# Performance work log

Hardware: AMD Instinct MI355X
Metric: run time of the kernel (lower is better)

The kernel has to match this reference:

```python
import jax, jax.numpy as jnp
import numpy as np

# Config matching init_kwargs: input_shape=(512,512,28), stride=2
M, N, L = 512, 512, 28
STRIDE = 2
B = 8


def setup_inputs() -> dict:
    key = jax.random.key(0)
    kx, kp = jax.random.split(key)
    x = jax.random.normal(kx, (B, L, M, N), dtype=jnp.float32)
    # phi = (1 + sign(randn)) / 2  -> binary {0,1} mask of shape (M, N)
    phi = (jax.random.normal(kp, (M, N)) > 0).astype(jnp.float32)
    return {"x": x, "phi": phi}


def reference(x, phi):
    """CASSI forward: get_transpose(get_measurement(x, phi), phi, mask_mul=True).

    x:   (b, L, M, N) hyperspectral cube
    phi: (M, N) coded aperture, broadcast across L bands
    """
    b, l, m, n = x.shape
    n_out = n + STRIDE * (l - 1)

    # --- get_measurement: mask-multiply then per-band shift-and-accumulate ---
    y1 = x * phi[None, None, :, :]                      # (b, L, M, N)
    # column index each (band, col) lands in after dispersion shift
    scat_idx = (STRIDE * jnp.arange(l)[:, None] + jnp.arange(n)[None, :]).reshape(-1)  # (L*N,)
    y1f = y1.transpose(0, 2, 1, 3).reshape(b, m, l * n)  # (b, M, L*N)
    y2 = jnp.zeros((b, m, n_out), dtype=x.dtype).at[:, :, scat_idx].add(y1f)  # (b, M, Nout)
    # y_norm=False: no normalization

    # --- get_transpose: gather shifted windows (width = y.shape[-2] = M) ---
    gat_idx = STRIDE * jnp.arange(l)[:, None] + jnp.arange(m)[None, :]  # (L, M)
    xt = y2[:, :, gat_idx]             # (b, M, L, M)
    xt = jnp.moveaxis(xt, 2, 1)        # (b, L, M, M)
    return xt * phi[None, None, :, :]  # mask_mul=True
```

## Files before the change

### kernel.cpp

```cpp
#include <hip/hip_runtime.h>


#define M_DIM 512
#define N_DIM 512
#define L_DIM 28
#define B_DIM 8
#define MN_DIM (M_DIM * N_DIM)
#define NT 14
#define U_DIM 14

typedef float v2f __attribute__((ext_vector_type(2)));
typedef float v4f __attribute__((ext_vector_type(4)));

__global__ __launch_bounds__(256) void cassi_fwd_kernel(
    const float* __restrict__ x, const float* __restrict__ phi,
    float* __restrict__ out)
{
    __shared__ __align__(16) float sphi[2][N_DIM];
    __shared__ __align__(16) float sy2[2][576];

    const int tid = threadIdx.x;
    const int r   = tid >> 7;
    const int t   = tid & 127;
    const int bm  = blockIdx.x;
    const int b   = bm >> 8;
    const int m   = ((bm & 255) << 1) | r;

    const float* xrow = x + (size_t)b * L_DIM * MN_DIM + (size_t)m * N_DIM;

    v4f pq = *(const v4f*)(phi + (size_t)m * N_DIM + 4 * t);
    *(v4f*)&sphi[r][4 * t] = pq;
    __syncthreads();

    const float* sphif = &sphi[r][0];
    const bool lane0 = ((tid & 63) == 0);

    v4f acc  = {0.f, 0.f, 0.f, 0.f};
    v4f acct = {0.f, 0.f, 0.f, 0.f};

#pragma unroll
    for (int u = 0; u < U_DIM; ++u) {
        const int s  = t - u;
        const int sc = s < 0 ? 0 : s;
        const float* re = xrow + (size_t)(2 * u) * MN_DIM;
        const float* ro = xrow + (size_t)(2 * u + 1) * MN_DIM;
        v4f xe = *(const v4f*)(re + 4 * sc);
        v4f xo = *(const v4f*)(ro + 4 * sc);
        v4f P  = *(const v4f*)(sphif + 4 * sc);
        v4f ze = xe * P;
        v4f zo = xo * P;

        if (s >= 0) acc += ze;

        float lo0 = __shfl_up(zo.z, 1, 64);
        float lo1 = __shfl_up(zo.w, 1, 64);
        if (lane0 && s >= 1) {
            v2f xl = *(const v2f*)(ro + 4 * s - 2);
            v2f pl = *(const v2f*)(sphif + 4 * s - 2);
            lo0 = xl.x * pl.x;
            lo1 = xl.y * pl.y;
        }
        if (s >= 1) { acc.x += lo0;  acc.y += lo1; }
        if (s >= 0) { acc.z += zo.x; acc.w += zo.y; }

        if (t < NT) {
            if (u == t) {
                v2f xl = *(const v2f*)(ro + 510);
                v2f pl = *(const v2f*)(sphif + 510);
                acct.x += xl.x * pl.x;
                acct.y += xl.y * pl.y;
            } else if (u > t) {
                const int n0 = 512 + 4 * t - 4 * u;
                v4f xte = *(const v4f*)(re + n0);
                v4f Pt  = *(const v4f*)(sphif + n0);
                acct += xte * Pt;
                v2f xa = *(const v2f*)(ro + n0 - 2);
                v2f pa = *(const v2f*)(sphif + n0 - 2);
                v2f xb = *(const v2f*)(ro + n0);
                acct.x += xa.x * pa.x;
                acct.y += xa.y * pa.y;
                acct.z += xb.x * Pt.x;
                acct.w += xb.y * Pt.y;
            }
        }
    }

    *(v4f*)&sy2[r][4 * t] = acc;
    if (t < NT) *(v4f*)&sy2[r][512 + 4 * t] = acct;
    __syncthreads();

    float* orow = out + (size_t)b * L_DIM * MN_DIM + (size_t)m * N_DIM;
    const float* sy = &sy2[r][0];
#pragma unroll
    for (int l = 0; l < L_DIM; ++l) {
        v2f ya = *(const v2f*)(sy + 2 * l + 4 * t);
        v2f yb = *(const v2f*)(sy + 2 * l + 4 * t + 2);
        v4f o;
        o.x = pq.x * ya.x;
        o.y = pq.y * ya.y;
        o.z = pq.z * yb.x;
        o.w = pq.w * yb.y;
        __builtin_nontemporal_store(o, (v4f*)(orow + (size_t)l * MN_DIM + 4 * t));
    }
}

extern "C" void kernel_launch(void* const* d_in, const int* in_sizes, int n_in,
                              void* d_out, int out_size, void* d_ws, size_t ws_size,
                              hipStream_t stream) {
    const float* x   = (const float*)d_in[0];
    const float* phi = (const float*)d_in[1];
    float* out       = (float*)d_out;
    cassi_fwd_kernel<<<dim3(B_DIM * M_DIM / 2), dim3(256), 0, stream>>>(x, phi, out);
}
```

Baseline: 391.7 us.

## Split band accumulation across half-blocks per row and replace shuffle with unaligned loads

Each block now handles a single row instead of two. Its two 128-thread halves each accumulate seven band pairs, combine the partial sums in shared memory, and then each write half of the 28 output bands. The odd-band shift now uses an unaligned 16-byte memcpy load rather than a cross-lane shuffle with a lane-0 fix-up. This doubles the grid and shortens each thread's serial load chain to raise memory-level parallelism, at the cost of an extra barrier and a shared-memory reduction.

```diff
diff --git a/kernel.cpp b/kernel.cpp
--- a/kernel.cpp
+++ b/kernel.cpp
@@ -7,7 +7,7 @@
 #define B_DIM 8
 #define MN_DIM (M_DIM * N_DIM)
 #define NT 14
-#define U_DIM 14
+#define UH 7
 
 typedef float v2f __attribute__((ext_vector_type(2)));
 typedef float v4f __attribute__((ext_vector_type(4)));
@@ -16,66 +16,69 @@
     const float* __restrict__ x, const float* __restrict__ phi,
     float* __restrict__ out)
 {
-    __shared__ __align__(16) float sphi[2][N_DIM];
-    __shared__ __align__(16) float sy2[2][576];
+    __shared__ __align__(16) float sphi[N_DIM];
+    __shared__ __align__(16) float psum[2][576];
 
     const int tid = threadIdx.x;
-    const int r   = tid >> 7;
+    const int h   = tid >> 7;
     const int t   = tid & 127;
     const int bm  = blockIdx.x;
-    const int b   = bm >> 8;
-    const int m   = ((bm & 255) << 1) | r;
+    const int b   = bm >> 9;
+    const int m   = bm & 511;
 
     const float* xrow = x + (size_t)b * L_DIM * MN_DIM + (size_t)m * N_DIM;
 
     v4f pq = *(const v4f*)(phi + (size_t)m * N_DIM + 4 * t);
-    *(v4f*)&sphi[r][4 * t] = pq;
+    if (h == 0) *(v4f*)&sphi[4 * t] = pq;
     __syncthreads();
-
-    const float* sphif = &sphi[r][0];
-    const bool lane0 = ((tid & 63) == 0);
 
     v4f acc  = {0.f, 0.f, 0.f, 0.f};
     v4f acct = {0.f, 0.f, 0.f, 0.f};
 
+    const int u0 = h * UH;
+
 #pragma unroll
-    for (int u = 0; u < U_DIM; ++u) {
+    for (int uu = 0; uu < UH; ++uu) {
+        const int u  = u0 + uu;
         const int s  = t - u;
-        const int sc = s < 0 ? 0 : s;
+        const int ec = s < 0 ? 0 : 4 * s;
+        const int od = 4 * s - 2;
+        const int oc = od < 0 ? 0 : od;
         const float* re = xrow + (size_t)(2 * u) * MN_DIM;
         const float* ro = xrow + (size_t)(2 * u + 1) * MN_DIM;
-        v4f xe = *(const v4f*)(re + 4 * sc);
-        v4f xo = *(const v4f*)(ro + 4 * sc);
-        v4f P  = *(const v4f*)(sphif + 4 * sc);
-        v4f ze = xe * P;
-        v4f zo = xo * P;
 
-        if (s >= 0) acc += ze;
+        v4f xe = *(const v4f*)(re + ec);
+        v4f P  = *(const v4f*)(&sphi[ec]);
+        if (s >= 0) acc += xe * P;
 
-        float lo0 = __shfl_up(zo.z, 1, 64);
-        float lo1 = __shfl_up(zo.w, 1, 64);
-        if (lane0 && s >= 1) {
-            v2f xl = *(const v2f*)(ro + 4 * s - 2);
-            v2f pl = *(const v2f*)(sphif + 4 * s - 2);
-            lo0 = xl.x * pl.x;
-            lo1 = xl.y * pl.y;
+        v4f xo;
+        __builtin_memcpy(&xo, ro + oc, 16);
+        v2f pl = *(const v2f*)(&sphi[oc]);
+        const bool ge1 = (s >= 1);
+        if (ge1) {
+            acc.x += xo.x * pl.x;
+            acc.y += xo.y * pl.y;
         }
-        if (s >= 1) { acc.x += lo0;  acc.y += lo1; }
-        if (s >= 0) { acc.z += zo.x; acc.w += zo.y; }
+        float za = ge1 ? xo.z : xo.x;
+        float zb = ge1 ? xo.w : xo.y;
+        if (s >= 0) {
+            acc.z += za * P.x;
+            acc.w += zb * P.y;
+        }
 
         if (t < NT) {
             if (u == t) {
-                v2f xl = *(const v2f*)(ro + 510);
-                v2f pl = *(const v2f*)(sphif + 510);
-                acct.x += xl.x * pl.x;
-                acct.y += xl.y * pl.y;
+                v2f xl  = *(const v2f*)(ro + 510);
+                v2f plt = *(const v2f*)(&sphi[510]);
+                acct.x += xl.x * plt.x;
+                acct.y += xl.y * plt.y;
             } else if (u > t) {
                 const int n0 = 512 + 4 * t - 4 * u;
                 v4f xte = *(const v4f*)(re + n0);
-                v4f Pt  = *(const v4f*)(sphif + n0);
+                v4f Pt  = *(const v4f*)(&sphi[n0]);
                 acct += xte * Pt;
                 v2f xa = *(const v2f*)(ro + n0 - 2);
-                v2f pa = *(const v2f*)(sphif + n0 - 2);
+                v2f pa = *(const v2f*)(&sphi[n0 - 2]);
                 v2f xb = *(const v2f*)(ro + n0);
                 acct.x += xa.x * pa.x;
                 acct.y += xa.y * pa.y;
@@ -85,14 +88,20 @@
         }
     }
 
-    *(v4f*)&sy2[r][4 * t] = acc;
-    if (t < NT) *(v4f*)&sy2[r][512 + 4 * t] = acct;
+    *(v4f*)&psum[h][4 * t] = acc;
+    if (t < NT) *(v4f*)&psum[h][512 + 4 * t] = acct;
+    __syncthreads();
+
+    for (int i = tid; i < 568; i += 256)
+        psum[0][i] += psum[1][i];
     __syncthreads();
 
     float* orow = out + (size_t)b * L_DIM * MN_DIM + (size_t)m * N_DIM;
-    const float* sy = &sy2[r][0];
+    const float* sy = &psum[0][0];
+    const int l0 = h * 14;
 #pragma unroll
-    for (int l = 0; l < L_DIM; ++l) {
+    for (int j = 0; j < 14; ++j) {
+        const int l = l0 + j;
         v2f ya = *(const v2f*)(sy + 2 * l + 4 * t);
         v2f yb = *(const v2f*)(sy + 2 * l + 4 * t + 2);
         v4f o;
@@ -110,5 +119,5 @@
     const float* x   = (const float*)d_in[0];
     const float* phi = (const float*)d_in[1];
     float* out       = (float*)d_out;
-    cassi_fwd_kernel<<<dim3(B_DIM * M_DIM / 2), dim3(256), 0, stream>>>(x, phi, out);
+    cassi_fwd_kernel<<<dim3(B_DIM * M_DIM), dim3(256), 0, stream>>>(x, phi, out);
 }
```

Result: slower. 405.7 us (+3.6%).
